# Kernel optimization log

Measured on AMD Instinct MI355X. Metric: run time of the kernel, lower is better.

Reference implementation:

```python
import jax, jax.numpy as jnp
import numpy as np

N = 100000
E = 1600000
IN_FEATS = 128
HIDDEN = 128
CLASSES = 64


def setup_inputs() -> dict:
    key = jax.random.key(0)
    ks = jax.random.split(key, 8)
    features = jax.random.normal(ks[0], (N, IN_FEATS), dtype=jnp.float32)
    edge_index = jax.random.randint(ks[1], (2, E), 0, N, dtype=jnp.int64 if jax.config.jax_enable_x64 else jnp.int32)
    # Glorot-init weights like PyG's GCNConv.lin, zero bias
    def glorot(k, fan_in, fan_out):
        lim = (6.0 / (fan_in + fan_out)) ** 0.5
        return jax.random.uniform(k, (fan_in, fan_out), dtype=jnp.float32, minval=-lim, maxval=lim)
    return {
        "features": features,
        "edge_index": edge_index,
        "W1": glorot(ks[2], IN_FEATS, HIDDEN), "b1": jnp.zeros((HIDDEN,), jnp.float32),
        "W2": glorot(ks[3], HIDDEN, HIDDEN), "b2": jnp.zeros((HIDDEN,), jnp.float32),
        "W3": glorot(ks[4], HIDDEN, CLASSES), "b3": jnp.zeros((CLASSES,), jnp.float32),
    }


def _gcn_conv(x, W, b, row, col, deg_norm_row, deg_norm_col):
    # x: [N, d_in] -> [N, d_out]. PyG GCNConv: linear first, then normalized aggregation, then bias.
    xw = x @ W                                   # [N, d_out]
    norm = deg_norm_row * deg_norm_col          # [E]
    msg = norm[:, None] * xw[row]               # gather from source nodes
    out = jax.ops.segment_sum(msg, col, num_segments=N)  # scatter-add to dst
    return out + b


def reference(features, edge_index, W1, b1, W2, b2, W3, b3):
    row, col = edge_index[0], edge_index[1]  # source -> target
    # gcn_norm with add_self_loops=False, unit edge weights: deg over dst nodes
    deg = jax.ops.segment_sum(jnp.ones((E,), features.dtype), col, num_segments=N)
    dinv = jnp.where(deg > 0, jax.lax.rsqrt(jnp.maximum(deg, 1.0)), 0.0)
    dn_row, dn_col = dinv[row], dinv[col]
    h = jax.nn.relu(_gcn_conv(features, W1, b1, row, col, dn_row, dn_col))
    h = jax.nn.relu(_gcn_conv(h, W2, b2, row, col, dn_row, dn_col))
    h = jax.nn.relu(_gcn_conv(h, W3, b3, row, col, dn_row, dn_col))
    return h
```

## Files before the change

### kernel.cpp

```cpp
#include <hip/hip_runtime.h>

#define ALIGNUP(x) (((x) + 255) & ~(size_t)255)
#define ABLK 256
#define BSHIFT 9

typedef _Float16 f16x8 __attribute__((ext_vector_type(8)));
typedef float f32x4 __attribute__((ext_vector_type(4)));


__global__ void bucket_hist_kernel(const int* __restrict__ col, unsigned* __restrict__ gHist,
                                   int nE, int chunk) {
    __shared__ unsigned hist[256];
    const int tid = threadIdx.x, blk = blockIdx.x;
    hist[tid] = 0;
    __syncthreads();
    const int e0 = blk * chunk, e1 = min(nE, e0 + chunk);
    for (int e = e0 + tid; e < e1; e += 256)
        atomicAdd(&hist[((unsigned)col[e]) >> BSHIFT], 1u);
    __syncthreads();
    gHist[tid * ABLK + blk] = hist[tid];
}

__global__ void bucket_scan_kernel(unsigned* __restrict__ g) {
    __shared__ unsigned ps[1024];
    const int tid = threadIdx.x;
    const int base = tid * 64;
    unsigned sum = 0;
    for (int k = 0; k < 64; ++k) sum += g[base + k];
    ps[tid] = sum;
    __syncthreads();
    for (int o = 1; o < 1024; o <<= 1) {
        unsigned t = tid >= o ? ps[tid - o] : 0u;
        __syncthreads();
        ps[tid] += t;
        __syncthreads();
    }
    unsigned run = ps[tid] - sum;
    for (int k = 0; k < 64; ++k) {
        unsigned v = g[base + k];
        g[base + k] = run;
        run += v;
    }
}

__global__ void bucket_scatter_kernel(const int* __restrict__ row, const int* __restrict__ col,
                                      const unsigned* __restrict__ gScan,
                                      unsigned* __restrict__ pairs, int nE, int chunk) {
    __shared__ unsigned basec[256];
    const int tid = threadIdx.x, blk = blockIdx.x;
    basec[tid] = gScan[tid * ABLK + blk];
    __syncthreads();
    const int e0 = blk * chunk, e1 = min(nE, e0 + chunk);
    for (int e = e0 + tid; e < e1; e += 256) {
        unsigned d = (unsigned)col[e];
        unsigned pos = atomicAdd(&basec[d >> BSHIFT], 1u);
        pairs[pos] = (((unsigned)row[e]) << BSHIFT) | (d & 511u);
    }
}

__global__ void bucket_sort_kernel(const unsigned* __restrict__ pairs,
                                   const unsigned* __restrict__ gScan,
                                   int* __restrict__ srcs, int* __restrict__ off,
                                   float* __restrict__ dinv, int nN, int nE) {
    __shared__ unsigned cnt[512], sc[512];
    const int tid = threadIdx.x, b = blockIdx.x;
    const unsigned s = gScan[b * ABLK];
    const unsigned t = (b + 1 < 256) ? gScan[(b + 1) * ABLK] : (unsigned)nE;
    cnt[tid] = 0;
    __syncthreads();
    for (unsigned i = s + tid; i < t; i += 512)
        atomicAdd(&cnt[pairs[i] & 511u], 1u);
    __syncthreads();
    const unsigned v = cnt[tid];
    sc[tid] = v;
    __syncthreads();
    for (int o = 1; o < 512; o <<= 1) {
        unsigned q = tid >= o ? sc[tid - o] : 0u;
        __syncthreads();
        sc[tid] += q;
        __syncthreads();
    }
    const unsigned excl = sc[tid] - v;
    const int node = b * 512 + tid;
    if (node < nN) {
        dinv[node] = v > 0 ? rsqrtf((float)v) : 0.f;
        off[node] = (int)(s + excl);
    }
    if (b == 0 && tid == 0) off[nN] = nE;
    sc[tid] = excl;
    __syncthreads();
    for (unsigned i = s + tid; i < t; i += 512) {
        unsigned p = pairs[i];
        unsigned pos = s + atomicAdd(&sc[p & 511u], 1u);
        srcs[pos] = (int)(p >> BSHIFT);
    }
}


template <int DOUT, bool AF32>
__launch_bounds__(256)
__global__ void gemm_mfma(const void* __restrict__ Xv, const float* __restrict__ W,
                          const float* __restrict__ dinv, _Float16* __restrict__ Y, int nrows) {
    constexpr int NTILE = DOUT / 16;
    __shared__ f16x8 Wf[NTILE * 4 * 64];
    const int tid = threadIdx.x;
    for (int idx = tid; idx < 128 * (DOUT / 4); idx += 256) {
        const int kk = idx / (DOUT / 4);
        const int n4 = (idx % (DOUT / 4)) * 4;
        const float4 w = ((const float4*)W)[idx];
        const int fk = kk >> 5, kb = (kk >> 3) & 3, e = kk & 7;
        const float wv[4] = {w.x, w.y, w.z, w.w};
#pragma unroll
        for (int d = 0; d < 4; ++d) {
            const int n = n4 + d;
            const int j = n >> 4;
            const int l = (n & 15) | (kb << 4);
            ((_Float16*)&Wf[(j * 4 + fk) * 64 + l])[e] = (_Float16)wv[d];
        }
    }
    __syncthreads();

    const int lane = tid & 63;
    const int wvid = tid >> 6;
    const int m = lane & 15;
    const int kb = lane >> 4;
    const int nchunks = (nrows + 63) >> 6;

    for (int c = blockIdx.x; c < nchunks; c += gridDim.x) {
        const int r0 = c * 64 + wvid * 16;
        const int arow = min(r0 + m, nrows - 1);
        f16x8 a[4];
        if constexpr (AF32) {
            const float* Xp = (const float*)Xv + (size_t)arow * 128 + kb * 8;
#pragma unroll
            for (int k = 0; k < 4; ++k) {
                const float4 x0 = *(const float4*)(Xp + k * 32);
                const float4 x1 = *(const float4*)(Xp + k * 32 + 4);
                f16x8 t;
                t[0] = (_Float16)x0.x; t[1] = (_Float16)x0.y;
                t[2] = (_Float16)x0.z; t[3] = (_Float16)x0.w;
                t[4] = (_Float16)x1.x; t[5] = (_Float16)x1.y;
                t[6] = (_Float16)x1.z; t[7] = (_Float16)x1.w;
                a[k] = t;
            }
        } else {
            const _Float16* Xp = (const _Float16*)Xv + (size_t)arow * 128 + kb * 8;
#pragma unroll
            for (int k = 0; k < 4; ++k) a[k] = *(const f16x8*)(Xp + k * 32);
        }
        f32x4 acc[NTILE];
#pragma unroll
        for (int j = 0; j < NTILE; ++j) acc[j] = (f32x4){0.f, 0.f, 0.f, 0.f};
#pragma unroll
        for (int k = 0; k < 4; ++k)
#pragma unroll
            for (int j = 0; j < NTILE; ++j)
                acc[j] = __builtin_amdgcn_mfma_f32_16x16x32_f16(
                             a[k], Wf[(j * 4 + k) * 64 + lane], acc[j], 0, 0, 0);
#pragma unroll
        for (int i = 0; i < 4; ++i) {
            const int r = r0 + kb * 4 + i;
            if (r < nrows) {
                const float dv = dinv[r];
#pragma unroll
                for (int j = 0; j < NTILE; ++j)
                    Y[(size_t)r * DOUT + j * 16 + m] = (_Float16)(acc[j][i] * dv);
            }
        }
    }
}


template <int DW, int LD, typename OT>
__launch_bounds__(256)
__global__ void gather_grp(const _Float16* __restrict__ XW, const int* __restrict__ off,
                           const int* __restrict__ srcs, const float* __restrict__ dinv,
                           const float* __restrict__ bias, OT* __restrict__ out, int nN) {
    constexpr int G   = DW / 8;
    constexpr int GPW = 64 / G;
    const int lane = threadIdx.x & 63;
    const int gl   = lane % G;
    const int grp  = lane / G;
    const int wid  = (blockIdx.x * blockDim.x + threadIdx.x) >> 6;
    const int nw   = (gridDim.x * blockDim.x) >> 6;

    for (int v0 = wid * GPW; v0 < nN; v0 += nw * GPW) {
        const int v   = v0 + grp;
        const bool act = v < nN;
        const int s0 = act ? off[v] : 0;
        const int s1 = act ? off[v + 1] : 0;
        float acc[8];
#pragma unroll
        for (int k = 0; k < 8; ++k) acc[k] = 0.f;

        int base = s0;
        while (base + G <= s1) {
            const int myidx = srcs[base + gl];
#pragma unroll
            for (int j = 0; j < G; ++j) {
                const int src = __shfl(myidx, grp * G + j);
                union { uint4 u; _Float16 h[8]; } cv;
                cv.u = *(const uint4*)(XW + (size_t)src * LD + gl * 8);
#pragma unroll
                for (int k = 0; k < 8; ++k) acc[k] += (float)cv.h[k];
            }
            base += G;
        }
        if (base < s1) {
            const int myidx = srcs[min(base + gl, s1 - 1)];
            const int rem = s1 - base;
            for (int j = 0; j < rem; ++j) {
                const int src = __shfl(myidx, grp * G + j);
                union { uint4 u; _Float16 h[8]; } cv;
                cv.u = *(const uint4*)(XW + (size_t)src * LD + gl * 8);
#pragma unroll
                for (int k = 0; k < 8; ++k) acc[k] += (float)cv.h[k];
            }
        }

        if (act) {
            const float dv = dinv[v];
            const float4 b0 = ((const float4*)bias)[gl * 2];
            const float4 b1 = ((const float4*)bias)[gl * 2 + 1];
            float o[8];
            o[0] = fmaxf(dv * acc[0] + b0.x, 0.f);
            o[1] = fmaxf(dv * acc[1] + b0.y, 0.f);
            o[2] = fmaxf(dv * acc[2] + b0.z, 0.f);
            o[3] = fmaxf(dv * acc[3] + b0.w, 0.f);
            o[4] = fmaxf(dv * acc[4] + b1.x, 0.f);
            o[5] = fmaxf(dv * acc[5] + b1.y, 0.f);
            o[6] = fmaxf(dv * acc[6] + b1.z, 0.f);
            o[7] = fmaxf(dv * acc[7] + b1.w, 0.f);
            if constexpr (sizeof(OT) == 2) {
                union { uint4 u; _Float16 h[8]; } ov;
#pragma unroll
                for (int k = 0; k < 8; ++k) ov.h[k] = (_Float16)o[k];
                *(uint4*)((_Float16*)out + (size_t)v * LD + gl * 8) = ov.u;
            } else {
                float* op = (float*)out + (size_t)v * LD + gl * 8;
                *(float4*)op       = make_float4(o[0], o[1], o[2], o[3]);
                *(float4*)(op + 4) = make_float4(o[4], o[5], o[6], o[7]);
            }
        }
    }
}

extern "C" void kernel_launch(void* const* d_in, const int* in_sizes, int n_in,
                              void* d_out, int out_size, void* d_ws, size_t ws_size,
                              hipStream_t stream) {
    const float* feats = (const float*)d_in[0];
    const int*   ei    = (const int*)d_in[1];
    const float* W1    = (const float*)d_in[2];
    const float* b1    = (const float*)d_in[3];
    const float* W2    = (const float*)d_in[4];
    const float* b2    = (const float*)d_in[5];
    const float* W3    = (const float*)d_in[6];
    const float* b3    = (const float*)d_in[7];

    const int N = in_sizes[0] / 128;
    const int E = in_sizes[1] / 2;
    const int* row = ei;
    const int* col = ei + E;

    char* p = (char*)d_ws;
    unsigned* gHist = (unsigned*)p; p += ALIGNUP((size_t)256 * ABLK * 4);
    float*     dinv = (float*)p;    p += ALIGNUP((size_t)N * 4);
    int*       off  = (int*)p;      p += ALIGNUP((size_t)(N + 1) * 4);
    int*       srcs = (int*)p;      p += ALIGNUP((size_t)E * 4);
    _Float16*  bufW = (_Float16*)p; p += ALIGNUP((size_t)N * 128 * 2);
    _Float16*  bufX = (_Float16*)p;
    unsigned* pairs = (unsigned*)bufX;

    const int chunk = (E + ABLK - 1) / ABLK;
    const int NB    = (N + 511) >> BSHIFT;
    bucket_hist_kernel<<<ABLK, 256, 0, stream>>>(col, gHist, E, chunk);
    bucket_scan_kernel<<<1, 1024, 0, stream>>>(gHist);
    bucket_scatter_kernel<<<ABLK, 256, 0, stream>>>(row, col, gHist, pairs, E, chunk);
    bucket_sort_kernel<<<NB, 512, 0, stream>>>(pairs, gHist, srcs, off, dinv, N, E);

    const int NCH = (N + 63) / 64;
    const int GG  = NCH < 800 ? NCH : 800;
    const int GBg = (N + 31) / 32;

    gemm_mfma<128, true><<<GG, 256, 0, stream>>>(feats, W1, dinv, bufW, N);
    gather_grp<64, 128, _Float16><<<GBg, 256, 0, stream>>>(bufW,      off, srcs, dinv,
                                                           b1,      bufX,      N);
    gather_grp<64, 128, _Float16><<<GBg, 256, 0, stream>>>(bufW + 64, off, srcs, dinv,
                                                           b1 + 64, bufX + 64, N);
    gemm_mfma<128, false><<<GG, 256, 0, stream>>>(bufX, W2, dinv, bufW, N);
    gather_grp<64, 128, _Float16><<<GBg, 256, 0, stream>>>(bufW,      off, srcs, dinv,
                                                           b2,      bufX,      N);
    gather_grp<64, 128, _Float16><<<GBg, 256, 0, stream>>>(bufW + 64, off, srcs, dinv,
                                                           b2 + 64, bufX + 64, N);
    gemm_mfma<64, false><<<GG, 256, 0, stream>>>(bufX, W3, dinv, bufW, N);
    gather_grp<64, 64, float><<<GBg, 256, 0, stream>>>(bufW, off, srcs, dinv, b3,
                                                       (float*)d_out, N);
}
```

Baseline: 303.9 us.

## Pre-swizzle weights once globally; one-chunk-per-block GEMM; merge gather halves via grid y

Weight matrices are converted to fp16 and swizzled into MFMA fragment layout by a small prep kernel, instead of every GEMM block rebuilding them in shared memory. The GEMM now launches one 64-row chunk per block with no grid-stride loop, and reads B fragments directly from global memory (cached in L2). The two half-width gather launches per layer become one launch with blockIdx.y choosing the half. This saves launch overhead and per-block LDS setup, at the cost of repeated global/L2 weight reads inside the MFMA loop.

```diff
diff --git a/kernel.cpp b/kernel.cpp
--- a/kernel.cpp
+++ b/kernel.cpp
@@ -97,87 +97,89 @@
 }
 
 
+template <int DOUT>
+__global__ void wf_prep_kernel(const float* __restrict__ W, f16x8* __restrict__ Wf) {
+    const int c = blockIdx.x * blockDim.x + threadIdx.x;
+    if (c >= DOUT * 16) return;
+    const int l = c & 63;
+    const int fk = (c >> 6) & 3;
+    const int j = c >> 8;
+    const int n = j * 16 + (l & 15);
+    const int kbase = fk * 32 + ((l >> 4) * 8);
+    f16x8 v;
+#pragma unroll
+    for (int e = 0; e < 8; ++e)
+        v[e] = (_Float16)W[(size_t)(kbase + e) * DOUT + n];
+    Wf[c] = v;
+}
+
+
 template <int DOUT, bool AF32>
 __launch_bounds__(256)
-__global__ void gemm_mfma(const void* __restrict__ Xv, const float* __restrict__ W,
+__global__ void gemm_mfma(const void* __restrict__ Xv, const f16x8* __restrict__ Wf,
                           const float* __restrict__ dinv, _Float16* __restrict__ Y, int nrows) {
     constexpr int NTILE = DOUT / 16;
-    __shared__ f16x8 Wf[NTILE * 4 * 64];
-    const int tid = threadIdx.x;
-    for (int idx = tid; idx < 128 * (DOUT / 4); idx += 256) {
-        const int kk = idx / (DOUT / 4);
-        const int n4 = (idx % (DOUT / 4)) * 4;
-        const float4 w = ((const float4*)W)[idx];
-        const int fk = kk >> 5, kb = (kk >> 3) & 3, e = kk & 7;
-        const float wv[4] = {w.x, w.y, w.z, w.w};
-#pragma unroll
-        for (int d = 0; d < 4; ++d) {
-            const int n = n4 + d;
-            const int j = n >> 4;
-            const int l = (n & 15) | (kb << 4);
-            ((_Float16*)&Wf[(j * 4 + fk) * 64 + l])[e] = (_Float16)wv[d];
-        }
-    }
-    __syncthreads();
-
-    const int lane = tid & 63;
-    const int wvid = tid >> 6;
+    const int lane = threadIdx.x & 63;
+    const int wvid = threadIdx.x >> 6;
     const int m = lane & 15;
     const int kb = lane >> 4;
-    const int nchunks = (nrows + 63) >> 6;
-
-    for (int c = blockIdx.x; c < nchunks; c += gridDim.x) {
-        const int r0 = c * 64 + wvid * 16;
-        const int arow = min(r0 + m, nrows - 1);
-        f16x8 a[4];
-        if constexpr (AF32) {
-            const float* Xp = (const float*)Xv + (size_t)arow * 128 + kb * 8;
-#pragma unroll
-            for (int k = 0; k < 4; ++k) {
-                const float4 x0 = *(const float4*)(Xp + k * 32);
-                const float4 x1 = *(const float4*)(Xp + k * 32 + 4);
-                f16x8 t;
-                t[0] = (_Float16)x0.x; t[1] = (_Float16)x0.y;
-                t[2] = (_Float16)x0.z; t[3] = (_Float16)x0.w;
-                t[4] = (_Float16)x1.x; t[5] = (_Float16)x1.y;
-                t[6] = (_Float16)x1.z; t[7] = (_Float16)x1.w;
-                a[k] = t;
-            }
-        } else {
-            const _Float16* Xp = (const _Float16*)Xv + (size_t)arow * 128 + kb * 8;
-#pragma unroll
-            for (int k = 0; k < 4; ++k) a[k] = *(const f16x8*)(Xp + k * 32);
-        }
-        f32x4 acc[NTILE];
-#pragma unroll
-        for (int j = 0; j < NTILE; ++j) acc[j] = (f32x4){0.f, 0.f, 0.f, 0.f};
-#pragma unroll
-        for (int k = 0; k < 4; ++k)
+    const int r0 = blockIdx.x * 64 + wvid * 16;
+    if (r0 >= nrows) return;
+    const int arow = min(r0 + m, nrows - 1);
+
+    f16x8 a[4];
+    if constexpr (AF32) {
+        const float* Xp = (const float*)Xv + (size_t)arow * 128 + kb * 8;
+#pragma unroll
+        for (int k = 0; k < 4; ++k) {
+            const float4 x0 = *(const float4*)(Xp + k * 32);
+            const float4 x1 = *(const float4*)(Xp + k * 32 + 4);
+            f16x8 t;
+            t[0] = (_Float16)x0.x; t[1] = (_Float16)x0.y;
+            t[2] = (_Float16)x0.z; t[3] = (_Float16)x0.w;
+            t[4] = (_Float16)x1.x; t[5] = (_Float16)x1.y;
+            t[6] = (_Float16)x1.z; t[7] = (_Float16)x1.w;
+            a[k] = t;
+        }
+    } else {
+        const _Float16* Xp = (const _Float16*)Xv + (size_t)arow * 128 + kb * 8;
+#pragma unroll
+        for (int k = 0; k < 4; ++k) a[k] = *(const f16x8*)(Xp + k * 32);
+    }
+
+    f32x4 acc[NTILE];
+#pragma unroll
+    for (int j = 0; j < NTILE; ++j) acc[j] = (f32x4){0.f, 0.f, 0.f, 0.f};
+#pragma unroll
+    for (int k = 0; k < 4; ++k)
+#pragma unroll
+        for (int j = 0; j < NTILE; ++j)
+            acc[j] = __builtin_amdgcn_mfma_f32_16x16x32_f16(
+                         a[k], Wf[(j * 4 + k) * 64 + lane], acc[j], 0, 0, 0);
+
+#pragma unroll
+    for (int i = 0; i < 4; ++i) {
+        const int r = r0 + kb * 4 + i;
+        if (r < nrows) {
+            const float dv = dinv[r];
 #pragma unroll
             for (int j = 0; j < NTILE; ++j)
-                acc[j] = __builtin_amdgcn_mfma_f32_16x16x32_f16(
-                             a[k], Wf[(j * 4 + k) * 64 + lane], acc[j], 0, 0, 0);
-#pragma unroll
-        for (int i = 0; i < 4; ++i) {
-            const int r = r0 + kb * 4 + i;
-            if (r < nrows) {
-                const float dv = dinv[r];
-#pragma unroll
-                for (int j = 0; j < NTILE; ++j)
-                    Y[(size_t)r * DOUT + j * 16 + m] = (_Float16)(acc[j][i] * dv);
-            }
-        }
-    }
-}
-
-
-template <int DW, int LD, typename OT>
+                Y[(size_t)r * DOUT + j * 16 + m] = (_Float16)(acc[j][i] * dv);
+        }
+    }
+}
+
+
+template <int LD, typename OT>
 __launch_bounds__(256)
 __global__ void gather_grp(const _Float16* __restrict__ XW, const int* __restrict__ off,
                            const int* __restrict__ srcs, const float* __restrict__ dinv,
                            const float* __restrict__ bias, OT* __restrict__ out, int nN) {
-    constexpr int G   = DW / 8;
-    constexpr int GPW = 64 / G;
+    constexpr int G = 8, GPW = 8;
+    const int half = blockIdx.y;
+    XW   += half * 64;
+    bias += half * 64;
+    out  += half * 64;
     const int lane = threadIdx.x & 63;
     const int gl   = lane % G;
     const int grp  = lane / G;
@@ -267,9 +269,16 @@
     float*     dinv = (float*)p;    p += ALIGNUP((size_t)N * 4);
     int*       off  = (int*)p;      p += ALIGNUP((size_t)(N + 1) * 4);
     int*       srcs = (int*)p;      p += ALIGNUP((size_t)E * 4);
+    f16x8*     wf1  = (f16x8*)p;    p += ALIGNUP((size_t)128 * 16 * 16);
+    f16x8*     wf2  = (f16x8*)p;    p += ALIGNUP((size_t)128 * 16 * 16);
+    f16x8*     wf3  = (f16x8*)p;    p += ALIGNUP((size_t)64 * 16 * 16);
     _Float16*  bufW = (_Float16*)p; p += ALIGNUP((size_t)N * 128 * 2);
     _Float16*  bufX = (_Float16*)p;
     unsigned* pairs = (unsigned*)bufX;
+
+    wf_prep_kernel<128><<<8, 256, 0, stream>>>(W1, wf1);
+    wf_prep_kernel<128><<<8, 256, 0, stream>>>(W2, wf2);
+    wf_prep_kernel<64><<<4, 256, 0, stream>>>(W3, wf3);
 
     const int chunk = (E + ABLK - 1) / ABLK;
     const int NB    = (N + 511) >> BSHIFT;
@@ -279,20 +288,15 @@
     bucket_sort_kernel<<<NB, 512, 0, stream>>>(pairs, gHist, srcs, off, dinv, N, E);
 
     const int NCH = (N + 63) / 64;
-    const int GG  = NCH < 800 ? NCH : 800;
     const int GBg = (N + 31) / 32;
 
-    gemm_mfma<128, true><<<GG, 256, 0, stream>>>(feats, W1, dinv, bufW, N);
-    gather_grp<64, 128, _Float16><<<GBg, 256, 0, stream>>>(bufW,      off, srcs, dinv,
-                                                           b1,      bufX,      N);
-    gather_grp<64, 128, _Float16><<<GBg, 256, 0, stream>>>(bufW + 64, off, srcs, dinv,
-                                                           b1 + 64, bufX + 64, N);
-    gemm_mfma<128, false><<<GG, 256, 0, stream>>>(bufX, W2, dinv, bufW, N);
-    gather_grp<64, 128, _Float16><<<GBg, 256, 0, stream>>>(bufW,      off, srcs, dinv,
-                                                           b2,      bufX,      N);
-    gather_grp<64, 128, _Float16><<<GBg, 256, 0, stream>>>(bufW + 64, off, srcs, dinv,
-                                                           b2 + 64, bufX + 64, N);
-    gemm_mfma<64, false><<<GG, 256, 0, stream>>>(bufX, W3, dinv, bufW, N);
-    gather_grp<64, 64, float><<<GBg, 256, 0, stream>>>(bufW, off, srcs, dinv, b3,
-                                                       (float*)d_out, N);
-}
+    gemm_mfma<128, true><<<NCH, 256, 0, stream>>>(feats, wf1, dinv, bufW, N);
+    gather_grp<128, _Float16><<<dim3(GBg, 2), 256, 0, stream>>>(bufW, off, srcs, dinv,
+                                                                b1, bufX, N);
+    gemm_mfma<128, false><<<NCH, 256, 0, stream>>>(bufX, wf2, dinv, bufW, N);
+    gather_grp<128, _Float16><<<dim3(GBg, 2), 256, 0, stream>>>(bufW, off, srcs, dinv,
+                                                                b2, bufX, N);
+    gemm_mfma<64, false><<<NCH, 256, 0, stream>>>(bufX, wf3, dinv, bufW, N);
+    gather_grp<64, float><<<dim3(GBg, 1), 256, 0, stream>>>(bufW, off, srcs, dinv, b3,
+                                                            (float*)d_out, N);
+}
```

Result: faster. 282.9 us (-6.9%).
